# Kernel tuning notes

Measured on AMD Instinct MI355X. Metric: run time of the kernel, lower is better.

The kernel has to match this reference:

```python
import jax, jax.numpy as jnp
import numpy as np

B, S, D_MODEL, N_HEADS = 4, 2048, 512, 2
D4 = D_MODEL * 4            # output dim of quaternion projections (2048)
HD = D4 // N_HEADS          # per-head dim (1024)
EPS = 1e-6


def quat_linear(x, W, b):
    """Hamilton-product quaternion linear.
    x: [..., 4*in_q] (quaternions interleaved r,i,j,k)
    W: [4, out_q, in_q] components (r,i,j,k); b: [4*out_q]
    returns [..., 4*out_q]
    """
    xq = x.reshape(x.shape[:-1] + (-1, 4))
    xr, xi, xj, xk = xq[..., 0], xq[..., 1], xq[..., 2], xq[..., 3]
    Wr, Wi, Wj, Wk = W[0], W[1], W[2], W[3]
    m = lambda a, M: jnp.einsum('...i,oi->...o', a, M)
    o_r = m(xr, Wr) - m(xi, Wi) - m(xj, Wj) - m(xk, Wk)
    o_i = m(xr, Wi) + m(xi, Wr) + m(xj, Wk) - m(xk, Wj)
    o_j = m(xr, Wj) - m(xi, Wk) + m(xj, Wr) + m(xk, Wi)
    o_k = m(xr, Wk) + m(xi, Wj) - m(xj, Wi) + m(xk, Wr)
    out = jnp.stack([o_r, o_i, o_j, o_k], axis=-1)
    return out.reshape(out.shape[:-2] + (-1,)) + b


def setup_inputs() -> dict:
    rng = jax.random.key(0)
    ks = jax.random.split(rng, 12)
    def w(k, out_q, in_q):
        return jax.random.normal(k, (4, out_q, in_q), jnp.float32) * (1.0 / np.sqrt(4.0 * in_q))
    in_q_small = D_MODEL // 4   # q/k/v projections: d_model reals -> d_model quaternions
    in_q_big = D4 // 4          # later projections: 4*d_model reals -> d_model quaternions
    zb = jnp.zeros((D4,), jnp.float32)
    return {
        'query': jax.random.normal(ks[0], (B, S, D_MODEL), jnp.float32),
        'key':   jax.random.normal(ks[1], (B, S, D_MODEL), jnp.float32),
        'value': jax.random.normal(ks[2], (B, S, D_MODEL), jnp.float32),
        'Wq': w(ks[3], D_MODEL, in_q_small), 'bq': zb,
        'Wk': w(ks[4], D_MODEL, in_q_small), 'bk': zb,
        'Wv': w(ks[5], D_MODEL, in_q_small), 'bv': zb,
        'alpha': jax.random.normal(ks[6], (D4,), jnp.float32) * 0.1,
        'Wint': w(ks[7], D_MODEL, in_q_big), 'bint': zb,
        'Wfin': w(ks[8], D_MODEL, in_q_big), 'bfin': zb,
        'Wout': w(ks[9], D_MODEL, in_q_big), 'bout': zb,
    }


def reference(query, key, value, Wq, bq, Wk, bk, Wv, bv, alpha,
              Wint, bint, Wfin, bfin, Wout, bout):
    Q = quat_linear(query, Wq, bq).reshape(B, S, N_HEADS, HD)
    K = quat_linear(key, Wk, bk).reshape(B, S, N_HEADS, HD)
    V = quat_linear(value, Wv, bv).reshape(B, S, N_HEADS, HD)

    # spectral attention: FFT correlation + adaptive spectral filter
    Qf = jnp.fft.fft(Q, axis=1)
    Kf = jnp.fft.fft(K, axis=1)
    corr = Qf * jnp.conj(Kf)                        # [B,S,H,HD] complex64
    freqs = jnp.abs(jnp.fft.fftfreq(S))             # [S]
    phase = jnp.arctan(jnp.log(freqs + EPS))        # [S]
    a = alpha.reshape(N_HEADS, HD)
    filt = jnp.exp(1j * (phase[:, None, None] * a[None, :, :]))  # [S,H,HD]
    attn_w = jnp.fft.ifft(corr * filt[None], axis=1).real        # [B,S,H,HD]
    attn = (attn_w * V).reshape(B, S, -1)           # [B,S,4*d_model]

    attn = quat_linear(attn, Wint, bint)
    attn = quat_linear(attn, Wfin, bfin)
    return quat_linear(attn, Wout, bout)            # [B,S,4*d_model]
```

## Files before the change

kernel.cpp:

```cpp
#include <hip/hip_runtime.h>
#include <hip/hip_bf16.h>
#include <cstdint>

typedef unsigned short u16;
typedef u16  u16x8 __attribute__((ext_vector_type(8)));
typedef short s16x8 __attribute__((ext_vector_type(8)));
typedef float f32x4 __attribute__((ext_vector_type(4)));

#define PI_F 3.14159265358979323846f
#define PD(i) ((i) + 3 * ((i) >> 5))

static __device__ __forceinline__ u16 f2bf(float f) {
    union { float f; unsigned u; } v; v.f = f;
    unsigned r = v.u + 0x7fffu + ((v.u >> 16) & 1u);
    return (u16)(r >> 16);
}
static __device__ __forceinline__ float bf2f(u16 h) {
    union { unsigned u; float f; } v; v.u = ((unsigned)h) << 16;
    return v.f;
}

__device__ __forceinline__ void gl_lds16(const u16* g, u16* l) {
    __builtin_amdgcn_global_load_lds(
        (const __attribute__((address_space(1))) unsigned int*)g,
        (__attribute__((address_space(3))) unsigned int*)l, 16, 0, 0);
}

__device__ __forceinline__ void cvt_body(int blk, const float* __restrict__ in,
                                         u16* __restrict__ o) {
    int i = blk * 256 + threadIdx.x;
    float4 a = ((const float4*)in)[2 * i];
    float4 b = ((const float4*)in)[2 * i + 1];
    u16x8 vv;
    vv[0] = f2bf(a.x); vv[1] = f2bf(a.y); vv[2] = f2bf(a.z); vv[3] = f2bf(a.w);
    vv[4] = f2bf(b.x); vv[5] = f2bf(b.y); vv[6] = f2bf(b.z); vv[7] = f2bf(b.w);
    ((u16x8*)o)[i] = vv;
}

template<int LOGK>
__device__ __forceinline__ void e3_body(int blk, const float* __restrict__ W,
                                        u16* __restrict__ E) {
    const int K = 1 << LOGK;
    int idx = blk * 256 + threadIdx.x;
    int n = idx >> LOGK, k = idx & (K - 1);
    int o = n >> 2, c = n & 3, i = k >> 2, cp = k & 3;
    const int   qm[4][4] = {{0,1,2,3},{1,0,3,2},{2,3,0,1},{3,2,1,0}};
    const float qs[4][4] = {{1.f,-1.f,-1.f,-1.f},{1.f,1.f,1.f,-1.f},
                            {1.f,-1.f,1.f,1.f},{1.f,1.f,-1.f,1.f}};
    int in_q = K >> 2;
    float w = W[(size_t)qm[c][cp] * 512 * in_q + (size_t)o * in_q + i] * qs[c][cp];
    E[idx] = f2bf(w);
}

__device__ __forceinline__ void tabs_body(int blk, float2* __restrict__ gws,
                                          float* __restrict__ ph) {
    int i = blk * 256 + threadIdx.x;
    if (i < 292) {
        int off, denom;
        if (i < 4)       { off = 0;  denom = 16;   }
        else if (i < 36) { off = 4;  denom = 128;  }
        else             { off = 36; denom = 1024; }
        float a = (-PI_F) * (float)(i - off) / (float)denom;
        gws[i] = make_float2(cosf(a), sinf(a));
    }
    if (i <= 1024) {
        ph[i] = atanf(logf((float)i * (1.0f / 2048.0f) + 1e-6f));
    }
}

__global__ __launch_bounds__(256) void fat_prep(
        const float* __restrict__ query, const float* __restrict__ key,
        const float* __restrict__ value, u16* __restrict__ Acvt,
        const float* __restrict__ Wq, const float* __restrict__ Wk,
        const float* __restrict__ Wv, u16* __restrict__ Eq,
        u16* __restrict__ Ek, u16* __restrict__ Ev,
        const float* __restrict__ Wint, const float* __restrict__ Wfin,
        const float* __restrict__ Wout, u16* __restrict__ Eint,
        u16* __restrict__ Efin, u16* __restrict__ Eout,
        float2* __restrict__ gws, float* __restrict__ pht) {
    int b = blockIdx.x;
    if (b < 6144) {
        int ten = b >> 11, r = b & 2047;
        const float* in = (ten == 0) ? query : (ten == 1) ? key : value;
        cvt_body(r, in, Acvt + (size_t)ten * 8192 * 512);
    } else if (b < 18432) {
        int rb = b - 6144;
        int y = rb >> 12, r = rb & 4095;
        e3_body<9>(r, (y == 0) ? Wq : (y == 1) ? Wk : Wv,
                   (y == 0) ? Eq : (y == 1) ? Ek : Ev);
    } else if (b < 67584) {
        int rb = b - 18432;
        int y = rb >> 14, r = rb & 16383;
        e3_body<11>(r, (y == 0) ? Wint : (y == 1) ? Wfin : Wout,
                    (y == 0) ? Eint : (y == 1) ? Efin : Eout);
    } else {
        tabs_body(b - 67584, gws, pht);
    }
}

__global__ __launch_bounds__(256) void matvec_E(const float* __restrict__ v,
                                                const u16* __restrict__ E,
                                                const float* __restrict__ badd,
                                                float* __restrict__ out) {
    int n    = (blockIdx.x * 256 + threadIdx.x) >> 6;
    int lane = threadIdx.x & 63;
    if (n >= 2048) return;
    const u16* row = E + (size_t)n * 2048;
    float s = 0.f;
    for (int j = lane; j < 2048; j += 64) s += v[j] * bf2f(row[j]);
#pragma unroll
    for (int o = 32; o; o >>= 1) s += __shfl_down(s, o, 64);
    if (lane == 0) out[n] = s + badd[n];
}

template<int K, int OUTMODE, int NBY>
__device__ __forceinline__ void gemm_body(int bid, u16* As, u16* Bs,
                                          const u16* __restrict__ A,
                                          const u16* __restrict__ E,
                                          const float* __restrict__ bias,
                                          void* __restrict__ outp) {
    const int t    = threadIdx.x;
    const int lane = t & 63, wave = t >> 6;
    const int wr   = wave >> 1, wc = wave & 1;
    const int lr   = lane & 15, kg = lane >> 4;
    const int l7   = lr & 7;

    constexpr int SPX = (4 * (NBY / 4)) / 8;
    const int xcd = bid & 7, p = bid >> 3;
    const int st  = xcd * SPX + (p >> 4);
    const int w   = p & 15;
    const int bx  = (st & 3) * 4 + (w & 3);
    const int by  = (st >> 2) * 4 + (w >> 2);
    const int m0  = by * 128;
    const int n0  = bx * 128;

    f32x4 acc[4][4];
#pragma unroll
    for (int i = 0; i < 4; ++i)
#pragma unroll
        for (int j = 0; j < 4; ++j) acc[i][j] = (f32x4){0.f, 0.f, 0.f, 0.f};

    const int arow = wr * 64 + lr;
    const int brow = wc * 64 + lr;

    for (int k0 = 0; k0 < K; k0 += 64) {
#pragma unroll
        for (int c = 0; c < 4; ++c) {
            int idx = t + c * 256;
            int row = idx >> 3, sl = idx & 7;
            int gsl = sl ^ (row & 7);
            gl_lds16(A + (size_t)(m0 + row) * K + k0 + gsl * 8, &As[idx * 8]);
            gl_lds16(E + (size_t)(n0 + row) * K + k0 + gsl * 8, &Bs[idx * 8]);
        }
        __syncthreads();
#pragma unroll
        for (int ks = 0; ks < 2; ++ks) {
            const int slot = (ks * 4 + kg) ^ l7;
            s16x8 av[4], bv[4];
#pragma unroll
            for (int mi = 0; mi < 4; ++mi)
                av[mi] = *(const s16x8*)&As[(arow + mi * 16) * 64 + slot * 8];
#pragma unroll
            for (int ni = 0; ni < 4; ++ni)
                bv[ni] = *(const s16x8*)&Bs[(brow + ni * 16) * 64 + slot * 8];
#pragma unroll
            for (int mi = 0; mi < 4; ++mi)
#pragma unroll
                for (int ni = 0; ni < 4; ++ni)
                    acc[mi][ni] = __builtin_amdgcn_mfma_f32_16x16x32_bf16(
                        av[mi], bv[ni], acc[mi][ni], 0, 0, 0);
        }
        __syncthreads();
    }

#pragma unroll
    for (int ni = 0; ni < 4; ++ni) {
        int n = n0 + wc * 64 + ni * 16 + lr;
        float bvl = bias ? bias[n] : 0.0f;
#pragma unroll
        for (int mi = 0; mi < 4; ++mi) {
#pragma unroll
            for (int r = 0; r < 4; ++r) {
                int m = m0 + wr * 64 + mi * 16 + kg * 4 + r;
                float val = acc[mi][ni][r] + bvl;
                if constexpr (OUTMODE == 0) {
                    ((u16*)outp)[(size_t)m * 2048 + n] = f2bf(val);
                } else if constexpr (OUTMODE == 1) {
                    ((float*)outp)[(size_t)m * 2048 + n] = val;
                } else {
                    int b = m >> 11, s = m & 2047;
                    ((u16*)outp)[((size_t)b * 2048 + n) * 2048 + s] = f2bf(val);
                }
            }
        }
    }
}

template<int K, int OUTMODE, int NBY>
__global__ __launch_bounds__(256) void gemm2(const u16* __restrict__ A,
                                             const u16* __restrict__ E,
                                             const float* __restrict__ bias,
                                             void* __restrict__ outp) {
    __shared__ u16 As[128 * 64];
    __shared__ u16 Bs[128 * 64];
    gemm_body<K, OUTMODE, NBY>(blockIdx.x, As, Bs, A, E, bias, outp);
}

__global__ __launch_bounds__(256) void gemm_fat1(const u16* __restrict__ Aq,
                                                 const u16* __restrict__ Eq,
                                                 const float* __restrict__ bq,
                                                 void* __restrict__ Qt,
                                                 const u16* __restrict__ Efin,
                                                 const u16* __restrict__ EintT,
                                                 void* __restrict__ T1T) {
    __shared__ u16 As[128 * 64];
    __shared__ u16 Bs[128 * 64];
    int bid = blockIdx.x;
    if (bid < 256)
        gemm_body<2048, 2, 16>(bid, As, Bs, Efin, EintT, nullptr, T1T);
    else
        gemm_body<512, 2, 64>(bid - 256, As, Bs, Aq, Eq, bq, Qt);
}

__global__ __launch_bounds__(256) void gemm_fat2(const u16* __restrict__ Ak,
                                                 const u16* __restrict__ Ek,
                                                 const float* __restrict__ bk,
                                                 void* __restrict__ Kt,
                                                 const u16* __restrict__ Eout,
                                                 const u16* __restrict__ T1T,
                                                 void* __restrict__ Ecomb) {
    __shared__ u16 As[128 * 64];
    __shared__ u16 Bs[128 * 64];
    int bid = blockIdx.x;
    if (bid < 256)
        gemm_body<2048, 0, 16>(bid, As, Bs, Eout, T1T, nullptr, Ecomb);
    else
        gemm_body<512, 2, 64>(bid - 256, As, Bs, Ak, Ek, bk, Kt);
}

template<int LH, int OFF>
__device__ __forceinline__ void r8pass(float* re, float* im,
                                       const float2* __restrict__ wt, int t) {
    constexpr int h = 1 << LH;
    __syncthreads();
    const int j  = t & (h - 1);
    const int i0 = ((t >> LH) << (LH + 3)) | j;
    const float2 w = wt[OFF + j];
    const float t2r = w.x * w.x - w.y * w.y;
    const float t2i = 2.f * w.x * w.y;
    const float t1r = t2r * t2r - t2i * t2i;
    const float t1i = 2.f * t2r * t2i;
    const float S = 0.70710678118654752f;
    const float Ac = S * (w.x + w.y);
    const float Bc = S * (w.y - w.x);

    float xr[8], xi[8];
    int p[8];
#pragma unroll
    for (int k = 0; k < 8; ++k) {
        p[k] = PD(i0 + k * h);
        xr[k] = re[p[k]]; xi[k] = im[p[k]];
    }
#pragma unroll
    for (int kp = 0; kp < 8; kp += 2) {
        float tr = t1r * xr[kp + 1] - t1i * xi[kp + 1];
        float ti = t1r * xi[kp + 1] + t1i * xr[kp + 1];
        float ar = xr[kp], ai = xi[kp];
        xr[kp] = ar + tr;     xi[kp] = ai + ti;
        xr[kp + 1] = ar - tr; xi[kp + 1] = ai - ti;
    }
#pragma unroll
    for (int q = 0; q < 2; ++q) {
        int b0 = q * 4;
        {
            float tr = t2r * xr[b0 + 2] - t2i * xi[b0 + 2];
            float ti = t2r * xi[b0 + 2] + t2i * xr[b0 + 2];
            float ar = xr[b0], ai = xi[b0];
            xr[b0] = ar + tr;     xi[b0] = ai + ti;
            xr[b0 + 2] = ar - tr; xi[b0 + 2] = ai - ti;
        }
        {
            float tr = t2i * xr[b0 + 3] + t2r * xi[b0 + 3];
            float ti = t2i * xi[b0 + 3] - t2r * xr[b0 + 3];
            float ar = xr[b0 + 1], ai = xi[b0 + 1];
            xr[b0 + 1] = ar + tr; xi[b0 + 1] = ai + ti;
            xr[b0 + 3] = ar - tr; xi[b0 + 3] = ai - ti;
        }
    }
    {
        float tr = w.x * xr[4] - w.y * xi[4];
        float ti = w.x * xi[4] + w.y * xr[4];
        float ar = xr[0], ai = xi[0];
        xr[0] = ar + tr; xi[0] = ai + ti;
        xr[4] = ar - tr; xi[4] = ai - ti;
    }
    {
        float tr = Ac * xr[5] - Bc * xi[5];
        float ti = Ac * xi[5] + Bc * xr[5];
        float ar = xr[1], ai = xi[1];
        xr[1] = ar + tr; xi[1] = ai + ti;
        xr[5] = ar - tr; xi[5] = ai - ti;
    }
    {
        float tr = w.y * xr[6] + w.x * xi[6];
        float ti = w.y * xi[6] - w.x * xr[6];
        float ar = xr[2], ai = xi[2];
        xr[2] = ar + tr; xi[2] = ai + ti;
        xr[6] = ar - tr; xi[6] = ai - ti;
    }
    {
        float tr = Bc * xr[7] + Ac * xi[7];
        float ti = Bc * xi[7] - Ac * xr[7];
        float ar = xr[3], ai = xi[3];
        xr[3] = ar + tr; xi[3] = ai + ti;
        xr[7] = ar - tr; xi[7] = ai - ti;
    }
#pragma unroll
    for (int k = 0; k < 8; ++k) { re[p[k]] = xr[k]; im[p[k]] = xi[k]; }
}

__device__ void fft2048(float* re, float* im, const float2* __restrict__ wt, int t) {
    __syncthreads();
#pragma unroll
    for (int u = 0; u < 2; ++u) {
        int i0 = (t + u * 256) << 2;
        int p0 = PD(i0);
        float x0r = re[p0],     x0i = im[p0];
        float x1r = re[p0 + 1], x1i = im[p0 + 1];
        float x2r = re[p0 + 2], x2i = im[p0 + 2];
        float x3r = re[p0 + 3], x3i = im[p0 + 3];
        float ar = x0r + x1r, ai = x0i + x1i;
        float br = x0r - x1r, bi = x0i - x1i;
        float cr = x2r + x3r, ci = x2i + x3i;
        float dr = x2r - x3r, di = x2i - x3i;
        re[p0]     = ar + cr; im[p0]     = ai + ci;
        re[p0 + 2] = ar - cr; im[p0 + 2] = ai - ci;
        re[p0 + 1] = br + di; im[p0 + 1] = bi - dr;
        re[p0 + 3] = br - di; im[p0 + 3] = bi + dr;
    }
    r8pass<2, 0>(re, im, wt, t);
    r8pass<5, 4>(re, im, wt, t);
    r8pass<8, 36>(re, im, wt, t);
    __syncthreads();
}

__device__ void spectral_body(int sbid, float* zre, float* zim, float2* wt,
                              const u16* __restrict__ Qt,
                              const u16* __restrict__ Kt,
                              u16* __restrict__ Wt,
                              const float* __restrict__ alpha,
                              const float2* __restrict__ gws,
                              const float* __restrict__ gph) {
    const int t  = threadIdx.x;
    const int b  = sbid >> 10;
    const int cp = sbid & 1023;
    const int c0 = cp * 2;
    const size_t base0 = ((size_t)b * 2048 + c0) * 2048;
    const size_t base1 = base0 + 2048;

    for (int i = t; i < 292; i += 256) wt[i] = gws[i];

    float ph[4];
    float PH1r[4], PH1i[4], PH2r[4], PH2i[4];
    float ph24 = 0.f, PH24_1 = 0.f, PH24_2 = 0.f;

#pragma unroll
    for (int ch = 0; ch < 2; ++ch) {
        const size_t base = ch ? base1 : base0;
        const u16* Qp = Qt + base;
        const u16* Kp = Kt + base;
        __syncthreads();
#pragma unroll
        for (int u = 0; u < 8; ++u) {
            int s = t + u * 256;
            int r = __brev((unsigned)s) >> 21;
            zre[PD(r)] = bf2f(Qp[s]);
            zim[PD(r)] = bf2f(Kp[s]);
        }
        fft2048(zre, zim, wt, t);
        const float ac = alpha[c0 + ch];
#pragma unroll
        for (int u = 0; u < 4; ++u) {
            int k = t + u * 256;
            int m = (2048 - k) & 2047;
            float ar = zre[PD(k)], ai = zim[PD(k)];
            float br = zre[PD(m)], bi = zim[PD(m)];
            float qr = 0.5f * (ar + br), qi = 0.5f * (ai - bi);
            float kr = 0.5f * (ai + bi), ki = 0.5f * (br - ar);
            float cr = qr * kr + qi * ki;
            float ci = qi * kr - qr * ki;
            if (ch == 0) ph[u] = gph[min(k, 2048 - k)];
            float fr, fi;
            __sincosf(ph[u] * ac, &fi, &fr);
            float Pkr = cr * fr - ci * fi, Pki = cr * fi + ci * fr;
            float qr2 = 0.5f * (br + ar), qi2 = 0.5f * (bi - ai);
            float kr2 = 0.5f * (bi + ai), ki2 = 0.5f * (ar - br);
            float cr2 = qr2 * kr2 + qi2 * ki2;
            float ci2 = qi2 * kr2 - qr2 * ki2;
            float Pmr = cr2 * fr - ci2 * fi, Pmi = cr2 * fi + ci2 * fr;
            float hr = 0.5f * (Pkr + Pmr), hi = 0.5f * (Pki - Pmi);
            if (ch == 0) { PH1r[u] = hr; PH1i[u] = hi; }
            else         { PH2r[u] = hr; PH2i[u] = hi; }
        }
        if (t == 0) {
            float ar = zre[PD(1024)], ai = zim[PD(1024)];
            float cr = ar * ai;
            if (ch == 0) ph24 = gph[1024];
            float fr, fi;
            __sincosf(ph24 * ac, &fi, &fr);
            if (ch == 0) PH24_1 = cr * fr; else PH24_2 = cr * fr;
        }
    }

    __syncthreads();
#pragma unroll
    for (int u = 0; u < 4; ++u) {
        int k = t + u * 256;
        int m = (2048 - k) & 2047;
        int rk = __brev((unsigned)k) >> 21;
        int rm = __brev((unsigned)m) >> 21;
        zre[PD(rk)] = PH1r[u] - PH2i[u];
        zim[PD(rk)] = PH1i[u] + PH2r[u];
        zre[PD(rm)] = PH1r[u] + PH2i[u];
        zim[PD(rm)] = PH2r[u] - PH1i[u];
    }
    if (t == 0) {
        zre[PD(1)] = PH24_1;
        zim[PD(1)] = PH24_2;
    }
    fft2048(zre, zim, wt, t);

#pragma unroll
    for (int u = 0; u < 8; ++u) {
        int s = t + u * 256;
        int j = (2048 - s) & 2047;
        Wt[base0 + s] = f2bf(zre[PD(j)] * (1.0f / 2048.0f));
        Wt[base1 + s] = f2bf(zim[PD(j)] * (1.0f / 2048.0f));
    }
}

__global__ __launch_bounds__(256) void fat_specv(const u16* __restrict__ Qt,
                                                 const u16* __restrict__ Kt,
                                                 u16* __restrict__ Wt,
                                                 const float* __restrict__ alpha,
                                                 const float2* __restrict__ gws,
                                                 const float* __restrict__ gph,
                                                 const u16* __restrict__ Av,
                                                 const u16* __restrict__ Ev,
                                                 const float* __restrict__ bvb,
                                                 void* __restrict__ Vt) {
    __shared__ __align__(16) char smem[32768];
    int bid = blockIdx.x;
    if (bid % 5 == 4) {
        gemm_body<512, 2, 64>(bid / 5, (u16*)smem, (u16*)(smem + 16384),
                              Av, Ev, bvb, Vt);
    } else {
        int sbid = (bid / 5) * 4 + (bid % 5);
        spectral_body(sbid, (float*)smem, (float*)(smem + 8960),
                      (float2*)(smem + 17920), Qt, Kt, Wt, alpha, gws, gph);
    }
}

__global__ __launch_bounds__(256) void transpose_k(const u16* __restrict__ in,
                                                   u16* __restrict__ out) {
    __shared__ u16 tile[32][33];
    int b = blockIdx.z;
    int c0 = blockIdx.x * 32, s0 = blockIdx.y * 32;
    int tx = threadIdx.x, ty = threadIdx.y;
#pragma unroll
    for (int dy = 0; dy < 32; dy += 8)
        tile[ty + dy][tx] = in[((size_t)b * 2048 + c0 + ty + dy) * 2048 + s0 + tx];
    __syncthreads();
#pragma unroll
    for (int dy = 0; dy < 32; dy += 8)
        out[((size_t)b * 2048 + s0 + ty + dy) * 2048 + c0 + tx] = tile[tx][ty + dy];
}

__global__ __launch_bounds__(256) void transpose_mul(const u16* __restrict__ W,
                                                     const u16* __restrict__ V,
                                                     u16* __restrict__ out) {
    __shared__ u16 tile[32][33];
    int b = blockIdx.z;
    int c0 = blockIdx.x * 32, s0 = blockIdx.y * 32;
    int tx = threadIdx.x, ty = threadIdx.y;
#pragma unroll
    for (int dy = 0; dy < 32; dy += 8) {
        size_t idx = ((size_t)b * 2048 + c0 + ty + dy) * 2048 + s0 + tx;
        tile[ty + dy][tx] = f2bf(bf2f(W[idx]) * bf2f(V[idx]));
    }
    __syncthreads();
#pragma unroll
    for (int dy = 0; dy < 32; dy += 8)
        out[((size_t)b * 2048 + s0 + ty + dy) * 2048 + c0 + tx] = tile[tx][ty + dy];
}

extern "C" void kernel_launch(void* const* d_in, const int* in_sizes, int n_in,
                              void* d_out, int out_size, void* d_ws, size_t ws_size,
                              hipStream_t stream) {
    const float* query = (const float*)d_in[0];
    const float* key   = (const float*)d_in[1];
    const float* value = (const float*)d_in[2];
    const float* Wq    = (const float*)d_in[3];
    const float* bq    = (const float*)d_in[4];
    const float* Wk    = (const float*)d_in[5];
    const float* bk    = (const float*)d_in[6];
    const float* Wv    = (const float*)d_in[7];
    const float* bv    = (const float*)d_in[8];
    const float* alpha = (const float*)d_in[9];
    const float* Wint  = (const float*)d_in[10];
    const float* bint  = (const float*)d_in[11];
    const float* Wfin  = (const float*)d_in[12];
    const float* bfin  = (const float*)d_in[13];
    const float* Wout  = (const float*)d_in[14];
    const float* bout  = (const float*)d_in[15];

    char* ws = (char*)d_ws;
    size_t off = 0;
    auto alloc = [&](size_t bytes) -> void* {
        void* p = ws + off;
        off += (bytes + 255) & ~(size_t)255;
        return p;
    };
    u16* Eq   = (u16*)alloc((size_t)2048 * 512 * 2);
    u16* Ek   = (u16*)alloc((size_t)2048 * 512 * 2);
    u16* Ev   = (u16*)alloc((size_t)2048 * 512 * 2);
    u16* Eint = (u16*)alloc((size_t)2048 * 2048 * 2);
    u16* Efin = (u16*)alloc((size_t)2048 * 2048 * 2);
    u16* Eout = (u16*)alloc((size_t)2048 * 2048 * 2);
    u16* EintT= (u16*)alloc((size_t)2048 * 2048 * 2);
    u16* T1T  = (u16*)alloc((size_t)2048 * 2048 * 2);
    u16* Qt   = (u16*)alloc((size_t)4 * 2048 * 2048 * 2);
    u16* Kt   = (u16*)alloc((size_t)4 * 2048 * 2048 * 2);
    u16* Vt   = (u16*)alloc((size_t)4 * 2048 * 2048 * 2);
    u16* attn = (u16*)alloc((size_t)8192 * 2048 * 2);
    float2* gws = (float2*)alloc(292 * 8);
    float*  pht = (float*)alloc(1025 * 4);
    float*  bv1 = (float*)alloc(2048 * 4);
    float*  bv2 = (float*)alloc(2048 * 4);
    u16* Ecomb = Eint;
    u16* Wt    = Efin;
    u16* Aq = attn;
    u16* Ak = attn + (size_t)8192 * 512;
    u16* Av = attn + (size_t)8192 * 1024;

    fat_prep<<<67589, 256, 0, stream>>>(query, key, value, Aq,
                                        Wq, Wk, Wv, Eq, Ek, Ev,
                                        Wint, Wfin, Wout, Eint, Efin, Eout,
                                        gws, pht);

    dim3 gt1(64, 64, 1);
    transpose_k<<<gt1, dim3(32, 8), 0, stream>>>(Eint, EintT);

    gemm_fat1<<<1280, 256, 0, stream>>>(Aq, Eq, bq, Qt, Efin, EintT, T1T);
    gemm_fat2<<<1280, 256, 0, stream>>>(Ak, Ek, bk, Kt, Eout, T1T, Ecomb);

    matvec_E<<<512, 256, 0, stream>>>(bint, Efin, bfin, bv1);
    matvec_E<<<512, 256, 0, stream>>>(bv1,  Eout, bout, bv2);

    fat_specv<<<5120, 256, 0, stream>>>(Qt, Kt, Wt, alpha, gws, pht,
                                        Av, Ev, bv, Vt);

    dim3 gt(64, 64, 4);
    transpose_mul<<<gt, dim3(32, 8), 0, stream>>>(Wt, Vt, attn);

    gemm2<2048, 1, 64><<<1024, 256, 0, stream>>>(attn, Ecomb, bv2, (float*)d_out);
}
```

Before: 373.4 us.

## Merge Q/K projections into one launch and fold combined-weight GEMM into spectral kernel

New measurement: 362.2 us (median of 2 runs). 1.03x faster.

```diff
diff --git a/kernel.cpp b/kernel.cpp
--- a/kernel.cpp
+++ b/kernel.cpp
@@ -206,36 +206,29 @@
     gemm_body<K, OUTMODE, NBY>(blockIdx.x, As, Bs, A, E, bias, outp);
 }
 
-__global__ __launch_bounds__(256) void gemm_fat1(const u16* __restrict__ Aq,
+__global__ __launch_bounds__(256) void gemm_fatA(const u16* __restrict__ Aq,
                                                  const u16* __restrict__ Eq,
                                                  const float* __restrict__ bq,
                                                  void* __restrict__ Qt,
+                                                 const u16* __restrict__ Ak,
+                                                 const u16* __restrict__ Ek,
+                                                 const float* __restrict__ bk,
+                                                 void* __restrict__ Kt,
                                                  const u16* __restrict__ Efin,
                                                  const u16* __restrict__ EintT,
                                                  void* __restrict__ T1T) {
     __shared__ u16 As[128 * 64];
     __shared__ u16 Bs[128 * 64];
     int bid = blockIdx.x;
-    if (bid < 256)
+    if (bid < 256) {
         gemm_body<2048, 2, 16>(bid, As, Bs, Efin, EintT, nullptr, T1T);
-    else
-        gemm_body<512, 2, 64>(bid - 256, As, Bs, Aq, Eq, bq, Qt);
-}
-
-__global__ __launch_bounds__(256) void gemm_fat2(const u16* __restrict__ Ak,
-                                                 const u16* __restrict__ Ek,
-                                                 const float* __restrict__ bk,
-                                                 void* __restrict__ Kt,
-                                                 const u16* __restrict__ Eout,
-                                                 const u16* __restrict__ T1T,
-                                                 void* __restrict__ Ecomb) {
-    __shared__ u16 As[128 * 64];
-    __shared__ u16 Bs[128 * 64];
-    int bid = blockIdx.x;
-    if (bid < 256)
-        gemm_body<2048, 0, 16>(bid, As, Bs, Eout, T1T, nullptr, Ecomb);
-    else
-        gemm_body<512, 2, 64>(bid - 256, As, Bs, Ak, Ek, bk, Kt);
+    } else {
+        int pid = bid - 256;
+        if (pid < 1024)
+            gemm_body<512, 2, 64>(pid, As, Bs, Aq, Eq, bq, Qt);
+        else
+            gemm_body<512, 2, 64>(pid - 1024, As, Bs, Ak, Ek, bk, Kt);
+    }
 }
 
 template<int LH, int OFF>
@@ -448,9 +441,18 @@
                                                  const u16* __restrict__ Av,
                                                  const u16* __restrict__ Ev,
                                                  const float* __restrict__ bvb,
-                                                 void* __restrict__ Vt) {
+                                                 void* __restrict__ Vt,
+                                                 const u16* __restrict__ Eout,
+                                                 const u16* __restrict__ T1T,
+                                                 void* __restrict__ Ecomb) {
     __shared__ __align__(16) char smem[32768];
     int bid = blockIdx.x;
+    if (bid < 256) {
+        gemm_body<2048, 0, 16>(bid, (u16*)smem, (u16*)(smem + 16384),
+                               Eout, T1T, nullptr, Ecomb);
+        return;
+    }
+    bid -= 256;
     if (bid % 5 == 4) {
         gemm_body<512, 2, 64>(bid / 5, (u16*)smem, (u16*)(smem + 16384),
                               Av, Ev, bvb, Vt);
@@ -538,7 +540,7 @@
     float*  bv1 = (float*)alloc(2048 * 4);
     float*  bv2 = (float*)alloc(2048 * 4);
     u16* Ecomb = Eint;
-    u16* Wt    = Efin;
+    u16* Wt    = Qt;
     u16* Aq = attn;
     u16* Ak = attn + (size_t)8192 * 512;
     u16* Av = attn + (size_t)8192 * 1024;
@@ -551,14 +553,14 @@
     dim3 gt1(64, 64, 1);
     transpose_k<<<gt1, dim3(32, 8), 0, stream>>>(Eint, EintT);
 
-    gemm_fat1<<<1280, 256, 0, stream>>>(Aq, Eq, bq, Qt, Efin, EintT, T1T);
-    gemm_fat2<<<1280, 256, 0, stream>>>(Ak, Ek, bk, Kt, Eout, T1T, Ecomb);
+    gemm_fatA<<<2304, 256, 0, stream>>>(Aq, Eq, bq, Qt, Ak, Ek, bk, Kt,
+                                        Efin, EintT, T1T);
 
     matvec_E<<<512, 256, 0, stream>>>(bint, Efin, bfin, bv1);
     matvec_E<<<512, 256, 0, stream>>>(bv1,  Eout, bout, bv2);
 
-    fat_specv<<<5120, 256, 0, stream>>>(Qt, Kt, Wt, alpha, gws, pht,
-                                        Av, Ev, bv, Vt);
+    fat_specv<<<5376, 256, 0, stream>>>(Qt, Kt, Wt, alpha, gws, pht,
+                                        Av, Ev, bv, Vt, Eout, T1T, Ecomb);
 
     dim3 gt(64, 64, 4);
     transpose_mul<<<gt, dim3(32, 8), 0, stream>>>(Wt, Vt, attn);
```
